# Optimization experiments

Measured on AMD Instinct MI355X. Metric: run time of the kernel, lower is better.

The kernel has to match this reference:

```python
import jax, jax.numpy as jnp
import numpy as np
import math

L = 4096
D = 1280
H = 16
HD = D // H  # 80
NSEG = 4


def setup_inputs() -> dict:
    key = jax.random.key(0)
    ks = jax.random.split(key, 8)
    x = jax.random.normal(ks[0], (L, D), dtype=jnp.float32)
    cu_seqlens = jnp.array([0, 1024, 2048, 3072, 4096], dtype=jnp.int32)
    rotary_pos_emb = jax.random.uniform(ks[1], (L, HD // 2), dtype=jnp.float32) * (2 * math.pi)
    s = 1.0 / math.sqrt(D)
    W_qkv = jax.random.normal(ks[2], (3 * D, D), dtype=jnp.float32) * s
    b_qkv = jax.random.normal(ks[3], (3 * D,), dtype=jnp.float32) * 0.01
    W_proj = jax.random.normal(ks[4], (D, D), dtype=jnp.float32) * s
    b_proj = jax.random.normal(ks[5], (D,), dtype=jnp.float32) * 0.01
    return {"x": x, "cu_seqlens": cu_seqlens, "rotary_pos_emb": rotary_pos_emb,
            "W_qkv": W_qkv, "b_qkv": b_qkv, "W_proj": W_proj, "b_proj": b_proj}


def _rotary_half(t):
    t1, t2 = jnp.split(t, 2, axis=-1)
    return jnp.concatenate([-t2, t1], axis=-1)


def _apply_rope(t, freq):
    # t: (L, H, HD), freq: (L, HD/2)
    cos = jnp.concatenate([jnp.cos(freq), jnp.cos(freq)], axis=-1)[:, None, :]
    sin = jnp.concatenate([jnp.sin(freq), jnp.sin(freq)], axis=-1)[:, None, :]
    return t * cos + _rotary_half(t) * sin


def reference(x, cu_seqlens, rotary_pos_emb, W_qkv, b_qkv, W_proj, b_proj):
    seq_len = x.shape[0]
    qkv = (x @ W_qkv.T + b_qkv).reshape(seq_len, 3, H, HD)
    q, k, v = qkv[:, 0], qkv[:, 1], qkv[:, 2]  # each (L, H, HD)
    q = _apply_rope(q, rotary_pos_emb)
    k = _apply_rope(k, rotary_pos_emb)
    # scores: (H, L, L)
    scores = jnp.einsum('lhd,mhd->hlm', q, k) / math.sqrt(HD)
    # block-diagonal mask from cu_seqlens: same segment -> 0, else finfo.min
    seg = jnp.searchsorted(cu_seqlens, jnp.arange(seq_len, dtype=jnp.int32), side='right')  # (L,)
    same = seg[:, None] == seg[None, :]
    neg = jnp.finfo(scores.dtype).min
    scores = scores + jnp.where(same, jnp.array(0.0, scores.dtype), neg)[None, :, :]
    attn = jax.nn.softmax(scores.astype(jnp.float32), axis=-1).astype(q.dtype)
    out = jnp.einsum('hlm,mhd->lhd', attn, v).reshape(seq_len, D)
    return out @ W_proj.T + b_proj
```

## Files before the change

kernel.cpp:

```cpp
#include <hip/hip_runtime.h>
#include <hip/hip_bf16.h>
#include <math.h>

#define LL   4096
#define DD   1280
#define HH   16
#define HDD  80
#define QKVN (3 * DD)

typedef __attribute__((ext_vector_type(8))) short sv8;
typedef __attribute__((ext_vector_type(4))) short sv4;
typedef __attribute__((ext_vector_type(4))) float fv4;

#if __has_builtin(__builtin_amdgcn_mfma_f32_16x16x16bf16_1k)
#define MFMA16(a, b, c) __builtin_amdgcn_mfma_f32_16x16x16bf16_1k(a, b, c, 0, 0, 0)
#elif __has_builtin(__builtin_amdgcn_mfma_f32_16x16x16_bf16)
#define MFMA16(a, b, c) __builtin_amdgcn_mfma_f32_16x16x16_bf16(a, b, c, 0, 0, 0)
#else
__device__ static inline fv4 MFMA16(sv4, sv4, fv4 c) { return c; }
#endif

#if __has_builtin(__builtin_amdgcn_exp2f)
#define EXP2F(x) __builtin_amdgcn_exp2f(x)
#else
#define EXP2F(x) exp2f(x)
#endif

static __device__ __forceinline__ unsigned short f2bf(float f) {
  unsigned int u = __builtin_bit_cast(unsigned int, f);
  u += 0x7FFF + ((u >> 16) & 1);
  return (unsigned short)(u >> 16);
}
static __device__ __forceinline__ float bf2f(unsigned short b) {
  unsigned int u = ((unsigned int)b) << 16;
  return __builtin_bit_cast(float, u);
}
static __device__ __forceinline__ unsigned int cvt_pk_bf16(float lo, float hi) {
  __hip_bfloat162 h = __float22bfloat162_rn(make_float2(lo, hi));
  unsigned int u;
  __builtin_memcpy(&u, &h, 4);
  return u;
}

#define GLD_LDS(gsrc, ldst)                                                          \
  __builtin_amdgcn_global_load_lds(                                                  \
      (const __attribute__((address_space(1))) unsigned int*)(gsrc),                 \
      (__attribute__((address_space(3))) unsigned int*)(ldst), 16, 0, 0)

__global__ __launch_bounds__(256) void cast3_kernel(
    const float* __restrict__ x, const float* __restrict__ w1,
    const float* __restrict__ w2, unsigned short* __restrict__ xb,
    unsigned short* __restrict__ w1b, unsigned short* __restrict__ w2b) {
  const int n0 = LL * DD / 8, n1 = QKVN * DD / 8, n2 = DD * DD / 8;
  int i = blockIdx.x * 256 + threadIdx.x;
  const float* in; unsigned short* out; int j;
  if (i < n0)           { in = x;  out = xb;  j = i; }
  else if (i < n0 + n1) { in = w1; out = w1b; j = i - n0; }
  else if (i < n0 + n1 + n2) { in = w2; out = w2b; j = i - n0 - n1; }
  else return;
  const float4* p = (const float4*)(in + (size_t)j * 8);
  float4 v0 = p[0], v1 = p[1];
  union { sv8 v; unsigned int u[4]; } o;
  o.u[0] = cvt_pk_bf16(v0.x, v0.y);
  o.u[1] = cvt_pk_bf16(v0.z, v0.w);
  o.u[2] = cvt_pk_bf16(v1.x, v1.y);
  o.u[3] = cvt_pk_bf16(v1.z, v1.w);
  *(sv8*)(out + (size_t)j * 8) = o.v;
}

__global__ __launch_bounds__(512, 2) void gemm256_bf16_kernel(
    const unsigned short* __restrict__ A, const unsigned short* __restrict__ B,
    const float* __restrict__ bias, unsigned short* __restrict__ C,
    int M, int N, int K) {
  __shared__ __attribute__((aligned(16))) unsigned short As[3][256 * 32];
  __shared__ __attribute__((aligned(16))) unsigned short Bs[3][256 * 32];
  int tid = threadIdx.x, w = tid >> 6, lane = tid & 63;
  int g = lane >> 4, l15 = lane & 15;
  int wr = w >> 2, wc = w & 3;

  int bid = blockIdx.x;
  int wg = (bid & 7) * 30 + (bid >> 3);
  int bm = (wg / 15) * 256;
  int bn = (wg % 15) * 256;

  fv4 acc[8][4];
#pragma unroll
  for (int a = 0; a < 8; ++a)
#pragma unroll
    for (int b = 0; b < 4; ++b) acc[a][b] = (fv4){0.f, 0.f, 0.f, 0.f};

  auto STAGE = [&](int buf, int t) {
    int k0 = t * 32;
#pragma unroll
    for (int i = 0; i < 4; ++i) {
      int cid = w * 4 + i;
      int c = cid & 15;
      int row = c * 16 + (lane >> 2);
      int gsrc = (lane & 3) ^ ((row >> 1) & 3);
      const unsigned short* src = (cid < 16)
          ? A + (size_t)(bm + row) * K + k0 + gsrc * 8
          : B + (size_t)(bn + row) * K + k0 + gsrc * 8;
      unsigned short* dst = ((cid < 16) ? As[buf] : Bs[buf]) + c * 512;
      GLD_LDS(src, dst);
    }
  };

  const int NT = 40;
  int r = 0;
  STAGE(0, 0);
  STAGE(1, 1);
  for (int t = 0; t < NT; ++t) {
    if (t + 1 < NT) asm volatile("s_waitcnt vmcnt(4)" ::: "memory");
    else            asm volatile("s_waitcnt vmcnt(0)" ::: "memory");
    __builtin_amdgcn_sched_barrier(0);
    asm volatile("s_barrier" ::: "memory");
    int s2 = (r == 0) ? 2 : r - 1;
    if (t + 2 < NT) STAGE(s2, t + 2);

    const unsigned short* Ab = As[r];
    const unsigned short* Bb = Bs[r];
    sv8 af[8], bfr[4];
#pragma unroll
    for (int mt = 0; mt < 8; ++mt) {
      int row = wr * 128 + mt * 16 + l15;
      af[mt] = *(const sv8*)(Ab + row * 32 + ((g ^ ((row >> 1) & 3)) * 8));
    }
#pragma unroll
    for (int nt = 0; nt < 4; ++nt) {
      int row = wc * 64 + nt * 16 + l15;
      bfr[nt] = *(const sv8*)(Bb + row * 32 + ((g ^ ((row >> 1) & 3)) * 8));
    }
#pragma unroll
    for (int mt = 0; mt < 8; ++mt)
#pragma unroll
      for (int nt = 0; nt < 4; ++nt)
        acc[mt][nt] = __builtin_amdgcn_mfma_f32_16x16x32_bf16(af[mt], bfr[nt], acc[mt][nt], 0, 0, 0);
    r = (r == 2) ? 0 : r + 1;
  }

#pragma unroll
  for (int mt = 0; mt < 8; ++mt)
#pragma unroll
    for (int nt = 0; nt < 4; ++nt) {
      int n = bn + wc * 64 + nt * 16 + l15;
      float bv = bias[n];
#pragma unroll
      for (int rr = 0; rr < 4; ++rr) {
        int m = bm + wr * 128 + mt * 16 + 4 * g + rr;
        C[(size_t)m * N + n] = f2bf(acc[mt][nt][rr] + bv);
      }
    }
}

__global__ __launch_bounds__(256) void gemm_bf16_kernel(
    const unsigned short* __restrict__ A, const unsigned short* __restrict__ B,
    const float* __restrict__ bias, void* __restrict__ Cv,
    int M, int N, int K, int out_bf16) {
  __shared__ __attribute__((aligned(16))) unsigned short As[2][128 * 64];
  __shared__ __attribute__((aligned(16))) unsigned short Bs[2][128 * 64];
  int tid = threadIdx.x, w = tid >> 6, lane = tid & 63;
  int g = lane >> 4, l15 = lane & 15;
  int wr = w >> 1, wc = w & 1;
  int bm = blockIdx.y * 128, bn = blockIdx.x * 128;

  fv4 acc[4][4];
#pragma unroll
  for (int a = 0; a < 4; ++a)
#pragma unroll
    for (int b = 0; b < 4; ++b) acc[a][b] = (fv4){0.f, 0.f, 0.f, 0.f};

  auto STAGE = [&](int buf, int k0) {
#pragma unroll
    for (int i = 0; i < 4; ++i) {
      int c = w * 4 + i;
      int row = 8 * c + (lane >> 3);
      int cb = lane & 7;
      int gcol = k0 + ((cb ^ (row & 7)) * 8);
      GLD_LDS(A + (size_t)(bm + row) * K + gcol, As[buf] + c * 512);
      GLD_LDS(B + (size_t)(bn + row) * K + gcol, Bs[buf] + c * 512);
    }
  };

  int nt = K / 64, cur = 0;
  STAGE(0, 0);
  if (nt > 1) STAGE(1, 64);
  for (int t = 0; t < nt; ++t) {
    if (t + 1 < nt) asm volatile("s_waitcnt vmcnt(8)" ::: "memory");
    else            asm volatile("s_waitcnt vmcnt(0)" ::: "memory");
    __builtin_amdgcn_sched_barrier(0);
    asm volatile("s_barrier" ::: "memory");
    const unsigned short* Ab = As[cur];
    const unsigned short* Bb = Bs[cur];
#pragma unroll
    for (int s = 0; s < 2; ++s) {
      sv8 af[4], bf[4];
#pragma unroll
      for (int t4 = 0; t4 < 4; ++t4) {
        int ra = wr * 64 + t4 * 16 + l15;
        af[t4] = *(const sv8*)(Ab + ra * 64 + (((s * 4 + g) ^ (ra & 7)) * 8));
        int rb = wc * 64 + t4 * 16 + l15;
        bf[t4] = *(const sv8*)(Bb + rb * 64 + (((s * 4 + g) ^ (rb & 7)) * 8));
      }
#pragma unroll
      for (int mt = 0; mt < 4; ++mt)
#pragma unroll
        for (int nt2 = 0; nt2 < 4; ++nt2)
          acc[mt][nt2] = __builtin_amdgcn_mfma_f32_16x16x32_bf16(af[mt], bf[nt2], acc[mt][nt2], 0, 0, 0);
    }
    asm volatile("s_waitcnt lgkmcnt(0)" ::: "memory");
    asm volatile("s_barrier" ::: "memory");
    if (t + 2 < nt) STAGE(cur, (t + 2) * 64);
    cur ^= 1;
  }

  if (out_bf16) {
    unsigned short* C = (unsigned short*)Cv;
#pragma unroll
    for (int mt = 0; mt < 4; ++mt)
#pragma unroll
      for (int nt2 = 0; nt2 < 4; ++nt2)
#pragma unroll
        for (int r = 0; r < 4; ++r) {
          int m = bm + wr * 64 + mt * 16 + 4 * g + r;
          int n = bn + wc * 64 + nt2 * 16 + l15;
          C[(size_t)m * N + n] = f2bf(acc[mt][nt2][r] + bias[n]);
        }
  } else {
    float* C = (float*)Cv;
#pragma unroll
    for (int mt = 0; mt < 4; ++mt)
#pragma unroll
      for (int nt2 = 0; nt2 < 4; ++nt2)
#pragma unroll
        for (int r = 0; r < 4; ++r) {
          int m = bm + wr * 64 + mt * 16 + 4 * g + r;
          int n = bn + wc * 64 + nt2 * 16 + l15;
          C[(size_t)m * N + n] = acc[mt][nt2][r] + bias[n];
        }
  }
}

__global__ __launch_bounds__(192) void pack_qk_kernel(
    const unsigned short* __restrict__ qkvb, const float* __restrict__ freqs,
    unsigned short* __restrict__ Qb, unsigned short* __restrict__ Kmain,
    unsigned short* __restrict__ Ktail) {
  int l = blockIdx.x;
  __shared__ float cs[40], sn[40];
  if (threadIdx.x < 40) {
    float f = freqs[(size_t)l * 40 + threadIdx.x];
    cs[threadIdx.x] = cosf(f);
    sn[threadIdx.x] = sinf(f);
  }
  __syncthreads();
  int t = threadIdx.x;
  if (t >= 160) return;
  int which = t / 80;
  int rem   = t % 80;
  int h = rem / 5, pg = rem % 5;
  int d0 = pg * 8;
  const unsigned short* src = qkvb + (size_t)l * QKVN + which * DD + h * HDD;
  union { sv8 v; unsigned short u[8]; } A, B;
  A.v = *(const sv8*)(src + d0);
  B.v = *(const sv8*)(src + d0 + 40);
  float scale = which ? 1.0f : 0.16129822676f;
  float lo[8], hi[8];
#pragma unroll
  for (int j = 0; j < 8; ++j) {
    float c = cs[d0 + j], s = sn[d0 + j];
    float a = bf2f(A.u[j]), b = bf2f(B.u[j]);
    lo[j] = (a * c - b * s) * scale;
    hi[j] = (b * c + a * s) * scale;
  }
  union { sv8 v; unsigned int u[4]; } OL, OH;
#pragma unroll
  for (int j = 0; j < 4; ++j) {
    OL.u[j] = cvt_pk_bf16(lo[2 * j], lo[2 * j + 1]);
    OH.u[j] = cvt_pk_bf16(hi[2 * j], hi[2 * j + 1]);
  }
  if (which == 0) {
    unsigned short* dst = Qb + ((size_t)h * LL + l) * HDD;
    *(sv8*)(dst + d0) = OL.v;
    *(sv8*)(dst + d0 + 40) = OH.v;
  } else {
    unsigned short* km = Kmain + ((size_t)h * LL + l) * 64;
    *(sv8*)(km + pg * 8) = OL.v;
    int dh = d0 + 40;
    if (dh < 64) {
      *(sv8*)(km + dh) = OH.v;
    } else {
      int blk = l >> 6, key = l & 63;
      int tg0 = (dh - 64) >> 2;
      size_t base = (((size_t)h * 64 + blk) * 4);
      uint2 w0 = make_uint2(OH.u[0], OH.u[1]);
      uint2 w1 = make_uint2(OH.u[2], OH.u[3]);
      *(uint2*)(Ktail + ((base + tg0) * 64 + key) * 4)     = w0;
      *(uint2*)(Ktail + ((base + tg0 + 1) * 64 + key) * 4) = w1;
    }
  }
}

__global__ __launch_bounds__(256) void pack_v_kernel(
    const unsigned short* __restrict__ qkvb, unsigned short* __restrict__ Vp) {
  __shared__ unsigned short vb[HDD][72];
  int blk = blockIdx.x, h = blockIdx.y;
  int l0 = blk * 64;
  for (int idx = threadIdx.x; idx < 64 * HDD; idx += 256) {
    int l = idx / HDD, d = idx % HDD;
    vb[d][l] = qkvb[(size_t)(l0 + l) * QKVN + 2 * DD + h * HDD + d];
  }
  __syncthreads();
  unsigned short* dst = Vp + (((size_t)h * 64 + blk) * 1280) * 4;
  for (int idx = threadIdx.x; idx < 16 * HDD; idx += 256) {
    int ntg = idx / HDD, d = idx % HDD;
    uint2 v = *(const uint2*)(&vb[d][ntg * 4]);
    *(uint2*)(dst + ((size_t)ntg * HDD + d) * 4) = v;
  }
}

__global__ __launch_bounds__(256) void attn_mfma_kernel(
    const unsigned short* __restrict__ Qb,
    const unsigned short* __restrict__ Kmain,
    const unsigned short* __restrict__ Ktail,
    const unsigned short* __restrict__ Vp,
    const int* __restrict__ cu,
    unsigned short* __restrict__ outb) {
  __shared__ __attribute__((aligned(16))) unsigned short Ks[2][64 * 64];
  __shared__ __attribute__((aligned(16))) unsigned short Kt[2][4 * 64 * 4];
  __shared__ __attribute__((aligned(16))) unsigned short Vl[2][16 * 80 * 4];
  int tid = threadIdx.x, w = tid >> 6, lane = tid & 63;
  int g = lane >> 4, l15 = lane & 15;

  int bid = blockIdx.x;
  int sw = (bid & 7) * 128 + (bid >> 3);
  int h = sw >> 6;
  int q0 = (sw & 63) * 64;

  int s0 = 0, s1 = LL;
#pragma unroll
  for (int i = 0; i < 4; ++i) {
    int a = cu[i], b = cu[i + 1];
    if (q0 >= a && q0 < b) { s0 = a; s1 = b; }
  }

  int qrow = q0 + w * 16 + l15;
  const unsigned short* qp = Qb + ((size_t)h * LL + qrow) * HDD;
  sv8 aq[2];
#pragma unroll
  for (int s = 0; s < 2; ++s) aq[s] = *(const sv8*)(qp + s * 32 + g * 8);
  union { sv4 v; uint2 u2; } qt;
  qt.u2 = *(const uint2*)(qp + 64 + 4 * g);

  auto STAGE = [&](int buf, int kb) {
    int blk = kb >> 6;
#pragma unroll
    for (int i = 0; i < 5; ++i) {
      int cid = w + 4 * i;
      if (cid < 8) {
        int row = 8 * cid + (lane >> 3);
        int cb = lane & 7;
        GLD_LDS(Kmain + ((size_t)h * LL + kb + row) * 64 + ((cb ^ (row & 7)) * 8),
                Ks[buf] + cid * 512);
      } else if (cid < 10) {
        int tc = cid - 8;
        GLD_LDS(Ktail + ((((size_t)h * 64 + blk) * 256) + tc * 128 + 2 * lane) * 4,
                Kt[buf] + tc * 512);
      } else {
        int vc = cid - 10;
        GLD_LDS(Vp + ((((size_t)h * 64 + blk) * 1280) + vc * 128 + 2 * lane) * 4,
                Vl[buf] + vc * 512);
      }
    }
  };

  fv4 o[5];
#pragma unroll
  for (int dt = 0; dt < 5; ++dt) o[dt] = (fv4){0.f, 0.f, 0.f, 0.f};
  float lsum = 0.f;

  int cur = 0;
  STAGE(0, s0);
  if (s0 + 64 < s1) STAGE(1, s0 + 64);
  for (int kb = s0; kb < s1; kb += 64) {
    if (kb + 64 < s1) asm volatile("s_waitcnt vmcnt(5)" ::: "memory");
    else              asm volatile("s_waitcnt vmcnt(0)" ::: "memory");
    __builtin_amdgcn_sched_barrier(0);
    asm volatile("s_barrier" ::: "memory");
    const unsigned short* Kc = Ks[cur];
    const unsigned short* Ktc = Kt[cur];
    const unsigned short* Vc = Vl[cur];

    fv4 sf[4];
#pragma unroll
    for (int nt = 0; nt < 4; ++nt) sf[nt] = (fv4){0.f, 0.f, 0.f, 0.f};
#pragma unroll
    for (int s = 0; s < 2; ++s) {
#pragma unroll
      for (int nt = 0; nt < 4; ++nt) {
        int key = nt * 16 + l15;
        sv8 ak = *(const sv8*)(Kc + key * 64 + (((s * 4 + g) ^ (key & 7)) * 8));
        sf[nt] = __builtin_amdgcn_mfma_f32_16x16x32_bf16(ak, aq[s], sf[nt], 0, 0, 0);
      }
    }
#pragma unroll
    for (int nt = 0; nt < 4; ++nt) {
      sv4 akt = *(const sv4*)(Ktc + (g * 64 + nt * 16 + l15) * 4);
      sf[nt] = MFMA16(akt, qt.v, sf[nt]);
    }

#pragma unroll
    for (int nt = 0; nt < 4; ++nt) {
      float p0 = EXP2F(sf[nt][0]);
      float p1 = EXP2F(sf[nt][1]);
      float p2 = EXP2F(sf[nt][2]);
      float p3 = EXP2F(sf[nt][3]);
      lsum += (p0 + p1) + (p2 + p3);
      union { sv4 v; unsigned int u[2]; } pa;
      pa.u[0] = cvt_pk_bf16(p0, p1);
      pa.u[1] = cvt_pk_bf16(p2, p3);
#pragma unroll
      for (int dt = 0; dt < 5; ++dt) {
        sv4 vb4 = *(const sv4*)(Vc + ((nt * 4 + g) * 80 + dt * 16 + l15) * 4);
        o[dt] = MFMA16(pa.v, vb4, o[dt]);
      }
    }
    asm volatile("s_waitcnt lgkmcnt(0)" ::: "memory");
    asm volatile("s_barrier" ::: "memory");
    if (kb + 128 < s1) STAGE(cur, kb + 128);
    cur ^= 1;
  }

  lsum += __shfl_xor(lsum, 16);
  lsum += __shfl_xor(lsum, 32);
  float inv = 1.f / lsum;
#pragma unroll
  for (int r = 0; r < 4; ++r) {
    float invr = __shfl(inv, 4 * g + r);
    int row = q0 + w * 16 + 4 * g + r;
#pragma unroll
    for (int dt = 0; dt < 5; ++dt) {
      outb[(size_t)row * DD + h * HDD + dt * 16 + l15] = f2bf(o[dt][r] * invr);
    }
  }
}

extern "C" void kernel_launch(void* const* d_in, const int* in_sizes, int n_in,
                              void* d_out, int out_size, void* d_ws, size_t ws_size,
                              hipStream_t stream) {
  const float* x     = (const float*)d_in[0];
  const int*   cu    = (const int*)d_in[1];
  const float* rope  = (const float*)d_in[2];
  const float* Wqkv  = (const float*)d_in[3];
  const float* bqkv  = (const float*)d_in[4];
  const float* Wproj = (const float*)d_in[5];
  const float* bproj = (const float*)d_in[6];
  float* out = (float*)d_out;

  char* ws = (char*)d_ws;
  unsigned short* qkvb   = (unsigned short*)ws;
  unsigned short* attn_b = (unsigned short*)ws;
  unsigned short* xb     = (unsigned short*)(ws + 31457280);
  unsigned short* Wqkvb  = (unsigned short*)(ws + 41943040);
  unsigned short* Wprojb = (unsigned short*)(ws + 51773440);
  unsigned short* Kmain  = (unsigned short*)(ws + 55050240);
  unsigned short* Ktail  = (unsigned short*)(ws + 63438848);
  unsigned short* Vp     = (unsigned short*)(ws + 65536000);
  unsigned short* Qb     = xb;

  {
    int n8 = LL * DD / 8 + QKVN * DD / 8 + DD * DD / 8;
    cast3_kernel<<<(n8 + 255) / 256, 256, 0, stream>>>(x, Wqkv, Wproj, xb, Wqkvb, Wprojb);
  }

  gemm256_bf16_kernel<<<240, 512, 0, stream>>>(
      xb, Wqkvb, bqkv, qkvb, LL, QKVN, DD);

  pack_qk_kernel<<<LL, 192, 0, stream>>>(qkvb, rope, Qb, Kmain, Ktail);
  pack_v_kernel<<<dim3(LL / 64, HH), 256, 0, stream>>>(qkvb, Vp);

  attn_mfma_kernel<<<1024, 256, 0, stream>>>(Qb, Kmain, Ktail, Vp, cu, attn_b);

  gemm_bf16_kernel<<<dim3(DD / 128, LL / 128), 256, 0, stream>>>(
      attn_b, Wprojb, bproj, out, LL, DD, DD, 0);
}
```

Before: 137.8 us.

## Raise wave priority around MFMA blocks and stagger half-tile order across waves

Wraps the MFMA compute sections of the QKV GEMM, the generic GEMM and the attention loop in s_setprio(1)/s_setprio(0) with scheduling barriers. In the QKV GEMM the A-fragment loads and MFMAs are also split into two halves, and the order of the halves depends on the wave index, so waves interleave their LDS reads with the other waves' matrix math. This also reduces live A-fragment registers. The risk is that the sched barriers stop the compiler from interleaving loads with MFMAs inside a wave.

```diff
diff --git a/kernel.cpp b/kernel.cpp
--- a/kernel.cpp
+++ b/kernel.cpp
@@ -25,6 +25,9 @@
 #else
 #define EXP2F(x) exp2f(x)
 #endif
+
+#define SETPRIO(n) __builtin_amdgcn_s_setprio(n)
+#define SCHEDB()   __builtin_amdgcn_sched_barrier(0)
 
 static __device__ __forceinline__ unsigned short f2bf(float f) {
   unsigned int u = __builtin_bit_cast(unsigned int, f);
@@ -105,38 +108,52 @@
     }
   };
 
+#define GHALF(H)                                                              \
+  {                                                                           \
+    sv8 af[4];                                                                \
+    _Pragma("unroll")                                                         \
+    for (int mt = 0; mt < 4; ++mt) {                                          \
+      int row = wr * 128 + ((H) * 4 + mt) * 16 + l15;                         \
+      af[mt] = *(const sv8*)(Ab + row * 32 + ((g ^ ((row >> 1) & 3)) * 8));   \
+    }                                                                         \
+    SCHEDB();                                                                 \
+    SETPRIO(1);                                                               \
+    _Pragma("unroll")                                                         \
+    for (int mt = 0; mt < 4; ++mt)                                            \
+      _Pragma("unroll")                                                       \
+      for (int nt = 0; nt < 4; ++nt)                                          \
+        acc[(H) * 4 + mt][nt] = __builtin_amdgcn_mfma_f32_16x16x32_bf16(      \
+            af[mt], bfr[nt], acc[(H) * 4 + mt][nt], 0, 0, 0);                 \
+    SETPRIO(0);                                                               \
+    SCHEDB();                                                                 \
+  }
+
   const int NT = 40;
   int r = 0;
+  int ph0 = (w >> 2) & 1;
   STAGE(0, 0);
   STAGE(1, 1);
   for (int t = 0; t < NT; ++t) {
     if (t + 1 < NT) asm volatile("s_waitcnt vmcnt(4)" ::: "memory");
     else            asm volatile("s_waitcnt vmcnt(0)" ::: "memory");
-    __builtin_amdgcn_sched_barrier(0);
+    SCHEDB();
     asm volatile("s_barrier" ::: "memory");
     int s2 = (r == 0) ? 2 : r - 1;
     if (t + 2 < NT) STAGE(s2, t + 2);
 
     const unsigned short* Ab = As[r];
     const unsigned short* Bb = Bs[r];
-    sv8 af[8], bfr[4];
-#pragma unroll
-    for (int mt = 0; mt < 8; ++mt) {
-      int row = wr * 128 + mt * 16 + l15;
-      af[mt] = *(const sv8*)(Ab + row * 32 + ((g ^ ((row >> 1) & 3)) * 8));
-    }
+    sv8 bfr[4];
 #pragma unroll
     for (int nt = 0; nt < 4; ++nt) {
       int row = wc * 64 + nt * 16 + l15;
       bfr[nt] = *(const sv8*)(Bb + row * 32 + ((g ^ ((row >> 1) & 3)) * 8));
     }
-#pragma unroll
-    for (int mt = 0; mt < 8; ++mt)
-#pragma unroll
-      for (int nt = 0; nt < 4; ++nt)
-        acc[mt][nt] = __builtin_amdgcn_mfma_f32_16x16x32_bf16(af[mt], bfr[nt], acc[mt][nt], 0, 0, 0);
+    if (ph0 == 0) { GHALF(0); GHALF(1); }
+    else          { GHALF(1); GHALF(0); }
     r = (r == 2) ? 0 : r + 1;
   }
+#undef GHALF
 
 #pragma unroll
   for (int mt = 0; mt < 8; ++mt)
@@ -187,7 +204,7 @@
   for (int t = 0; t < nt; ++t) {
     if (t + 1 < nt) asm volatile("s_waitcnt vmcnt(8)" ::: "memory");
     else            asm volatile("s_waitcnt vmcnt(0)" ::: "memory");
-    __builtin_amdgcn_sched_barrier(0);
+    SCHEDB();
     asm volatile("s_barrier" ::: "memory");
     const unsigned short* Ab = As[cur];
     const unsigned short* Bb = Bs[cur];
@@ -201,11 +218,15 @@
         int rb = wc * 64 + t4 * 16 + l15;
         bf[t4] = *(const sv8*)(Bb + rb * 64 + (((s * 4 + g) ^ (rb & 7)) * 8));
       }
+      SCHEDB();
+      SETPRIO(1);
 #pragma unroll
       for (int mt = 0; mt < 4; ++mt)
 #pragma unroll
         for (int nt2 = 0; nt2 < 4; ++nt2)
           acc[mt][nt2] = __builtin_amdgcn_mfma_f32_16x16x32_bf16(af[mt], bf[nt2], acc[mt][nt2], 0, 0, 0);
+      SETPRIO(0);
+      SCHEDB();
     }
     asm volatile("s_waitcnt lgkmcnt(0)" ::: "memory");
     asm volatile("s_barrier" ::: "memory");
@@ -383,12 +404,13 @@
   for (int kb = s0; kb < s1; kb += 64) {
     if (kb + 64 < s1) asm volatile("s_waitcnt vmcnt(5)" ::: "memory");
     else              asm volatile("s_waitcnt vmcnt(0)" ::: "memory");
-    __builtin_amdgcn_sched_barrier(0);
+    SCHEDB();
     asm volatile("s_barrier" ::: "memory");
     const unsigned short* Kc = Ks[cur];
     const unsigned short* Ktc = Kt[cur];
     const unsigned short* Vc = Vl[cur];
 
+    SETPRIO(1);
     fv4 sf[4];
 #pragma unroll
     for (int nt = 0; nt < 4; ++nt) sf[nt] = (fv4){0.f, 0.f, 0.f, 0.f};
@@ -423,6 +445,7 @@
         o[dt] = MFMA16(pa.v, vb4, o[dt]);
       }
     }
+    SETPRIO(0);
     asm volatile("s_waitcnt lgkmcnt(0)" ::: "memory");
     asm volatile("s_barrier" ::: "memory");
     if (kb + 128 < s1) STAGE(cur, kb + 128);
```

Result: slower. 141.9 us (+2.9%).
